# Performance work log

Hardware: AMD Instinct MI355X
Metric: run time of the kernel (lower is better)

## Reference

```python
import jax, jax.numpy as jnp
import numpy as np

DIM = 1024
NUM_HEADS = 16
WINDOW_SIZE = 512
HEAD_DIM = DIM // NUM_HEADS
SCALE = HEAD_DIM ** (-0.5)


def setup_inputs() -> dict:
    key = jax.random.key(0)
    kq, kk, kv = jax.random.split(key, 3)
    shape = (2, NUM_HEADS, 2048, HEAD_DIM)
    q = jax.random.normal(kq, shape, dtype=jnp.float32)
    k = jax.random.normal(kk, shape, dtype=jnp.float32)
    v = jax.random.normal(kv, shape, dtype=jnp.float32)
    return {"q": q, "k": k, "v": v}


def reference(q, k, v):
    B, H, N, D = q.shape
    pos = jnp.arange(N)
    # causal + sliding window: col <= row and col >= row - w + 1
    window_mask = (pos[None, :] <= pos[:, None]) & (pos[None, :] >= pos[:, None] - WINDOW_SIZE + 1)  # (N, N)
    attn = jnp.einsum("bhnd,bhmd->bhnm", q, k) * SCALE  # (B, H, N, N)
    attn = jnp.where(window_mask[None, None], attn, -jnp.inf)
    attn = jax.nn.softmax(attn, axis=-1)
    attn = jnp.nan_to_num(attn, nan=0.0)
    return jnp.einsum("bhnm,bhmd->bhnd", attn, v)
```

## Files before the change

kernel.cpp:

```cpp
#include <hip/hip_runtime.h>
#include <math.h>


#define SEQ 2048
#define HD  64
#define LDR 72

typedef short short8 __attribute__((ext_vector_type(8)));
typedef float f32x4  __attribute__((ext_vector_type(4)));

static __device__ inline unsigned short f2bf(float f){
  union{float f; unsigned u;} un; un.f=f;
  return (unsigned short)((un.u + 0x7FFFu + ((un.u>>16)&1u))>>16);
}
static __device__ inline int swz(int row){ return (row&3)|(((row>>3)&1)<<2); }

static __device__ __forceinline__ void gll16(const unsigned short* g, unsigned short* l){
  __builtin_amdgcn_global_load_lds(
    (const __attribute__((address_space(1))) unsigned int*)(const void*)g,
    (__attribute__((address_space(3))) unsigned int*)(void*)l, 16, 0, 0);
}

__global__ __launch_bounds__(256) void swa_prep(
    const float* __restrict__ k, const float* __restrict__ v,
    unsigned short* __restrict__ Kb, unsigned short* __restrict__ Vtb)
{
  __shared__ unsigned short Vs[64*68];
  const int tid=threadIdx.x, bid=blockIdx.x;
  const long tbase=(long)bid*4096;
  const float C=0.18033688011112042f;

  #pragma unroll
  for(int i=0;i<2;++i){
    int id=i*256+tid, r=id>>3, lc=id&7;
    float4 f0=*(const float4*)(k+tbase+r*64+lc*8);
    float4 f1=*(const float4*)(k+tbase+r*64+lc*8+4);
    unsigned short hh[8];
    hh[0]=f2bf(f0.x*C); hh[1]=f2bf(f0.y*C); hh[2]=f2bf(f0.z*C); hh[3]=f2bf(f0.w*C);
    hh[4]=f2bf(f1.x*C); hh[5]=f2bf(f1.y*C); hh[6]=f2bf(f1.z*C); hh[7]=f2bf(f1.w*C);
    *(uint4*)(Kb+tbase+r*64+(long)((lc^swz(r))*8))=*(uint4*)hh;
  }
  #pragma unroll
  for(int i=0;i<2;++i){
    int id=i*256+tid, r=id>>3, c=id&7;
    int phys=(c^(r>>3))&7;
    float4 f0=*(const float4*)(v+tbase+r*64+c*8);
    float4 f1=*(const float4*)(v+tbase+r*64+c*8+4);
    ushort4 a,b;
    a.x=f2bf(f0.x); a.y=f2bf(f0.y); a.z=f2bf(f0.z); a.w=f2bf(f0.w);
    b.x=f2bf(f1.x); b.y=f2bf(f1.y); b.z=f2bf(f1.z); b.w=f2bf(f1.w);
    *(ushort4*)&Vs[r*68+phys*8]  =a;
    *(ushort4*)&Vs[r*68+phys*8+4]=b;
  }
  __syncthreads();
  #pragma unroll
  for(int i=0;i<2;++i){
    int id=i*256+tid, d=id>>3, lc=id&7;
    unsigned short t8[8];
    #pragma unroll
    for(int e=0;e<8;++e){
      int key=lc*8+e;
      int phys=((d>>3)^lc)&7;
      t8[e]=Vs[key*68 + phys*8 + (d&7)];
    }
    *(uint4*)(Vtb+tbase+d*64+(long)((lc^swz(d))*8))=*(uint4*)t8;
  }
}

__global__ __launch_bounds__(512) void swa_main(
    const float* __restrict__ q,
    const unsigned short* __restrict__ Kb,
    const unsigned short* __restrict__ Vtb,
    float* __restrict__ out)
{
  __shared__ unsigned short Ks[2][4096];
  __shared__ unsigned short Vsh[2][4096];

  const int tid=threadIdx.x, bid=blockIdx.x;
  const int mt=bid&15, bh=bid>>4, m0=mt*128;
  const long base=(long)bh*SEQ*HD;
  const int wv=tid>>6, lane=tid&63, quad=lane>>4, l16=lane&15;
  const int qrow=m0+wv*16+l16;
  const int h=wv>>2;

  short8 qa[2];
  {
    const float* qp=q+base+(long)qrow*HD+quad*8;
    #pragma unroll
    for(int kk=0;kk<2;++kk){
      float4 f0=*(const float4*)(qp+kk*32);
      float4 f1=*(const float4*)(qp+kk*32+4);
      short8 a;
      a[0]=(short)f2bf(f0.x); a[1]=(short)f2bf(f0.y);
      a[2]=(short)f2bf(f0.z); a[3]=(short)f2bf(f0.w);
      a[4]=(short)f2bf(f1.x); a[5]=(short)f2bf(f1.y);
      a[6]=(short)f2bf(f1.z); a[7]=(short)f2bf(f1.w);
      qa[kk]=a;
    }
  }

  const int rbase=8*(l16>>2)+(l16&3);
  const int swk=(l16&3)|(((l16>>2)&1)<<2);
  const int swv=(l16&3)|(((l16>>3)&1)<<2);
  int kaoff[2][4], vboff[2][4];
  #pragma unroll
  for(int kk=0;kk<2;++kk){
    #pragma unroll
    for(int nt=0;nt<4;++nt)
      kaoff[kk][nt]=(rbase+(nt&1)*4+(nt>>1)*32)*64+(((quad+4*kk)^swk)*8);
    #pragma unroll
    for(int dt=0;dt<4;++dt)
      vboff[kk][dt]=(dt*16+l16)*64+(((quad+4*kk)^swv)*8);
  }

  const unsigned short* Kt=Kb +(long)bh*32*4096;
  const unsigned short* Vt=Vtb+(long)bh*32*4096;
  const int seg=tid*8;

  f32x4 oacc[4];
  #pragma unroll
  for(int dt=0;dt<4;++dt) oacc[dt]=(f32x4){0.f,0.f,0.f,0.f};
  float lrun=0.f;

  const int Tb  =2*mt+1;
  const int Tlo =(2*mt>8)?(2*mt-8):0;
  const int myTb=2*mt+h;
  const int myTlo=(myTb>=8)?(myTb-8):0;
  const bool clip=(myTb>=8);

  gll16(Kt+(long)Tlo*4096+seg, &Ks[0][seg]);
  gll16(Vt+(long)Tlo*4096+seg, &Vsh[0][seg]);
  __syncthreads();

  for(int t=Tlo;t<=Tb;++t){
    const int buf=(t-Tlo)&1;
    if(t<Tb){
      gll16(Kt+(long)(t+1)*4096+seg, &Ks[buf^1][seg]);
      gll16(Vt+(long)(t+1)*4096+seg, &Vsh[buf^1][seg]);
    }
    if(t>=myTlo && t<=myTb){
      f32x4 sacc[4];
      #pragma unroll
      for(int nt=0;nt<4;++nt) sacc[nt]=(f32x4){0.f,0.f,0.f,0.f};
      #pragma unroll
      for(int kk=0;kk<2;++kk){
        #pragma unroll
        for(int nt=0;nt<4;++nt){
          short8 ka=*(const short8*)&Ks[buf][kaoff[kk][nt]];
          sacc[nt]=__builtin_amdgcn_mfma_f32_16x16x32_bf16(ka,qa[kk],sacc[nt],0,0,0);
        }
      }
      short8 vb[4][2];
      #pragma unroll
      for(int dt=0;dt<4;++dt)
        #pragma unroll
        for(int kk=0;kk<2;++kk)
          vb[dt][kk]=*(const short8*)&Vsh[buf][vboff[kk][dt]];

      unsigned short pb[16];
      const bool msk=(t==myTb)||(clip&&t==myTlo);
      if(msk){
        #pragma unroll
        for(int nt=0;nt<4;++nt){
          #pragma unroll
          for(int r=0;r<4;++r){
            float e=__builtin_amdgcn_exp2f(sacc[nt][r]);
            int key=t*64+8*quad+r+(nt&1)*4+(nt>>1)*32;
            bool valid=(key<=qrow)&&(key+511>=qrow);
            e=valid?e:0.f;
            lrun+=e;
            pb[nt*4+r]=f2bf(e);
          }
        }
      } else {
        #pragma unroll
        for(int nt=0;nt<4;++nt){
          #pragma unroll
          for(int r=0;r<4;++r){
            float e=__builtin_amdgcn_exp2f(sacc[nt][r]);
            lrun+=e;
            pb[nt*4+r]=f2bf(e);
          }
        }
      }
      short8 pa0,pa1;
      #pragma unroll
      for(int j=0;j<8;++j){ pa0[j]=(short)pb[j]; pa1[j]=(short)pb[8+j]; }
      #pragma unroll
      for(int dt=0;dt<4;++dt){
        oacc[dt]=__builtin_amdgcn_mfma_f32_16x16x32_bf16(pa0,vb[dt][0],oacc[dt],0,0,0);
        oacc[dt]=__builtin_amdgcn_mfma_f32_16x16x32_bf16(pa1,vb[dt][1],oacc[dt],0,0,0);
      }
    }
    __syncthreads();
  }

  lrun+=__shfl_xor(lrun,16);
  lrun+=__shfl_xor(lrun,32);
  float linv=1.0f/lrun;
  #pragma unroll
  for(int r=0;r<4;++r){
    float lr=__shfl(linv,quad*4+r);
    const int orow=m0+wv*16+quad*4+r;
    #pragma unroll
    for(int dt=0;dt<4;++dt)
      out[base+(long)orow*HD+dt*16+l16]=oacc[dt][r]*lr;
  }
}

__global__ __launch_bounds__(256) void swa_fwd(
    const float* __restrict__ q, const float* __restrict__ k,
    const float* __restrict__ v, float* __restrict__ out)
{
  __shared__ short Qs[64*LDR];
  __shared__ short Ps[64*LDR];
  __shared__ short Ksh[2][64*LDR];
  __shared__ short Vtr[2][HD*LDR];

  const int tid=threadIdx.x, bid=blockIdx.x;
  const int mtile=bid&31, bh=bid>>5, m0=mtile*64;
  const long base=(long)bh*SEQ*HD;
  const int wv=tid>>6, lane=tid&63, quad=lane>>4, l16=lane&15;
  const int dcol=lane;

  {
    const float4* qg=(const float4*)(q+base+(long)m0*HD);
    #pragma unroll
    for(int i=0;i<4;++i){
      int idx=i*256+tid, r=idx>>4, c4=idx&15;
      float4 f=qg[idx];
      ushort4 hh; hh.x=f2bf(f.x); hh.y=f2bf(f.y); hh.z=f2bf(f.z); hh.w=f2bf(f.w);
      *(ushort4*)&Qs[r*LDR+c4*4]=hh;
    }
  }
  const int tb=mtile, tlo=(tb>8)?(tb-8):0;
  float4 kreg[4]; float vcol[4][4];
  {
    const float4* kg=(const float4*)(k+base+(long)(tlo*64)*HD);
    const float*  vg=v+base+(long)(tlo*64)*HD;
    #pragma unroll
    for(int i=0;i<4;++i) kreg[i]=kg[i*256+tid];
    #pragma unroll
    for(int g=0;g<4;++g){ int r0=wv*4+g*16;
      #pragma unroll
      for(int j=0;j<4;++j) vcol[g][j]=vg[(r0+j)*HD+dcol]; }
  }
  __syncthreads();
  short8 qa[2];
  #pragma unroll
  for(int kk=0;kk<2;++kk)
    qa[kk]=*(const short8*)&Qs[(wv*16+l16)*LDR+kk*32+quad*8];
  {
    #pragma unroll
    for(int i=0;i<4;++i){
      int idx=i*256+tid, r=idx>>4, c4=idx&15;
      float4 fk=kreg[i];
      ushort4 hk; hk.x=f2bf(fk.x); hk.y=f2bf(fk.y); hk.z=f2bf(fk.z); hk.w=f2bf(fk.w);
      *(ushort4*)&Ksh[0][r*LDR+c4*4]=hk;
    }
    #pragma unroll
    for(int g=0;g<4;++g){ int r0=wv*4+g*16;
      ushort4 hv; hv.x=f2bf(vcol[g][0]); hv.y=f2bf(vcol[g][1]);
                  hv.z=f2bf(vcol[g][2]); hv.w=f2bf(vcol[g][3]);
      *(ushort4*)&Vtr[0][dcol*LDR+r0]=hv; }
  }
  float lrun[4]={0.f,0.f,0.f,0.f};
  f32x4 oacc[4];
  #pragma unroll
  for(int dt=0;dt<4;++dt) oacc[dt]=(f32x4){0.f,0.f,0.f,0.f};
  __syncthreads();

  for(int t=tlo;t<=tb;++t){
    const int buf=(t-tlo)&1, j0=t*64;
    f32x4 sacc[4];
    #pragma unroll
    for(int nt=0;nt<4;++nt) sacc[nt]=(f32x4){0.f,0.f,0.f,0.f};
    #pragma unroll
    for(int kk=0;kk<2;++kk){
      #pragma unroll
      for(int nt=0;nt<4;++nt){
        short8 kb=*(const short8*)&Ksh[buf][(nt*16+l16)*LDR+kk*32+quad*8];
        sacc[nt]=__builtin_amdgcn_mfma_f32_16x16x32_bf16(qa[kk],kb,sacc[nt],0,0,0);
      }
    }
    if(t<tb){
      const float4* kg=(const float4*)(k+base+(long)((t+1)*64)*HD);
      const float*  vg=v+base+(long)((t+1)*64)*HD;
      #pragma unroll
      for(int i=0;i<4;++i) kreg[i]=kg[i*256+tid];
      #pragma unroll
      for(int g=0;g<4;++g){ int r0=wv*4+g*16;
        #pragma unroll
        for(int j=0;j<4;++j) vcol[g][j]=vg[(r0+j)*HD+dcol]; }
    }
    #pragma unroll
    for(int r=0;r<4;++r){
      const int grr=m0+wv*16+quad*4+r;
      #pragma unroll
      for(int nt=0;nt<4;++nt){
        const int gc=j0+nt*16+l16;
        float e=exp2f(sacc[nt][r]*0.18033688011112042f);
        float p=((gc<=grr)&&(gc>=grr-511))?e:0.f;
        lrun[r]+=p;
        Ps[(wv*16+quad*4+r)*LDR+nt*16+l16]=(short)f2bf(p);
      }
    }
    __syncthreads();
    #pragma unroll
    for(int kk=0;kk<2;++kk){
      short8 pa=*(const short8*)&Ps[(wv*16+l16)*LDR+kk*32+quad*8];
      #pragma unroll
      for(int dt=0;dt<4;++dt){
        short8 vb=*(const short8*)&Vtr[buf][(dt*16+l16)*LDR+kk*32+quad*8];
        oacc[dt]=__builtin_amdgcn_mfma_f32_16x16x32_bf16(pa,vb,oacc[dt],0,0,0);
      }
    }
    if(t<tb){
      #pragma unroll
      for(int i=0;i<4;++i){
        int idx=i*256+tid, r=idx>>4, c4=idx&15;
        float4 fk=kreg[i];
        ushort4 hk; hk.x=f2bf(fk.x); hk.y=f2bf(fk.y); hk.z=f2bf(fk.z); hk.w=f2bf(fk.w);
        *(ushort4*)&Ksh[buf^1][r*LDR+c4*4]=hk;
      }
      #pragma unroll
      for(int g=0;g<4;++g){ int r0=wv*4+g*16;
        ushort4 hv; hv.x=f2bf(vcol[g][0]); hv.y=f2bf(vcol[g][1]);
                    hv.z=f2bf(vcol[g][2]); hv.w=f2bf(vcol[g][3]);
        *(ushort4*)&Vtr[buf^1][dcol*LDR+r0]=hv; }
    }
    __syncthreads();
  }
  #pragma unroll
  for(int r=0;r<4;++r){
    float s=lrun[r];
    s+=__shfl_xor(s,1); s+=__shfl_xor(s,2); s+=__shfl_xor(s,4); s+=__shfl_xor(s,8);
    lrun[r]=(s>0.f)?(1.f/s):0.f;
  }
  #pragma unroll
  for(int r=0;r<4;++r){
    const int row=m0+wv*16+quad*4+r;
    #pragma unroll
    for(int dt=0;dt<4;++dt)
      out[base+(long)row*HD+dt*16+l16]=oacc[dt][r]*lrun[r];
  }
}

extern "C" void kernel_launch(void* const* d_in, const int* in_sizes, int n_in,
                              void* d_out, int out_size, void* d_ws, size_t ws_size,
                              hipStream_t stream) {
  (void)in_sizes; (void)n_in; (void)out_size;
  const float* q=(const float*)d_in[0];
  const float* k=(const float*)d_in[1];
  const float* v=(const float*)d_in[2];
  float* o=(float*)d_out;
  const size_t NEED = 2ull*32*2048*64*2;
  if (ws_size>=NEED){
    unsigned short* Kb =(unsigned short*)d_ws;
    unsigned short* Vtb=Kb+32ull*2048*64;
    hipLaunchKernelGGL(swa_prep, dim3(1024), dim3(256), 0, stream, k, v, Kb, Vtb);
    hipLaunchKernelGGL(swa_main, dim3(512),  dim3(512), 0, stream, q, Kb, Vtb, o);
  } else {
    hipLaunchKernelGGL(swa_fwd, dim3(1024), dim3(256), 0, stream, q, k, v, o);
  }
}
```

Baseline: 110.0 us.

## Process two key tiles per barrier and split prep kernel into K and V blocks

The main attention loop now stages two 64-key tiles of K and V per double-buffered stage, which halves the number of __syncthreads barriers and issues larger batches of async global-to-LDS loads. LDS use grows to 64KB per block, which may limit occupancy. The prep kernel now launches separate blocks for K conversion and V transpose, doubling the grid so the two jobs run in parallel and only the V blocks need shared memory. The tile count per block is even (10 or 2*mt+2), so the pairing covers every tile.

```diff
diff --git a/kernel.cpp b/kernel.cpp
--- a/kernel.cpp
+++ b/kernel.cpp
@@ -25,45 +25,49 @@
     const float* __restrict__ k, const float* __restrict__ v,
     unsigned short* __restrict__ Kb, unsigned short* __restrict__ Vtb)
 {
-  __shared__ unsigned short Vs[64*68];
   const int tid=threadIdx.x, bid=blockIdx.x;
-  const long tbase=(long)bid*4096;
   const float C=0.18033688011112042f;
 
-  #pragma unroll
-  for(int i=0;i<2;++i){
-    int id=i*256+tid, r=id>>3, lc=id&7;
-    float4 f0=*(const float4*)(k+tbase+r*64+lc*8);
-    float4 f1=*(const float4*)(k+tbase+r*64+lc*8+4);
-    unsigned short hh[8];
-    hh[0]=f2bf(f0.x*C); hh[1]=f2bf(f0.y*C); hh[2]=f2bf(f0.z*C); hh[3]=f2bf(f0.w*C);
-    hh[4]=f2bf(f1.x*C); hh[5]=f2bf(f1.y*C); hh[6]=f2bf(f1.z*C); hh[7]=f2bf(f1.w*C);
-    *(uint4*)(Kb+tbase+r*64+(long)((lc^swz(r))*8))=*(uint4*)hh;
-  }
-  #pragma unroll
-  for(int i=0;i<2;++i){
-    int id=i*256+tid, r=id>>3, c=id&7;
-    int phys=(c^(r>>3))&7;
-    float4 f0=*(const float4*)(v+tbase+r*64+c*8);
-    float4 f1=*(const float4*)(v+tbase+r*64+c*8+4);
-    ushort4 a,b;
-    a.x=f2bf(f0.x); a.y=f2bf(f0.y); a.z=f2bf(f0.z); a.w=f2bf(f0.w);
-    b.x=f2bf(f1.x); b.y=f2bf(f1.y); b.z=f2bf(f1.z); b.w=f2bf(f1.w);
-    *(ushort4*)&Vs[r*68+phys*8]  =a;
-    *(ushort4*)&Vs[r*68+phys*8+4]=b;
-  }
-  __syncthreads();
-  #pragma unroll
-  for(int i=0;i<2;++i){
-    int id=i*256+tid, d=id>>3, lc=id&7;
-    unsigned short t8[8];
-    #pragma unroll
-    for(int e=0;e<8;++e){
-      int key=lc*8+e;
-      int phys=((d>>3)^lc)&7;
-      t8[e]=Vs[key*68 + phys*8 + (d&7)];
-    }
-    *(uint4*)(Vtb+tbase+d*64+(long)((lc^swz(d))*8))=*(uint4*)t8;
+  if(bid<1024){
+    const long tbase=(long)bid*4096;
+    #pragma unroll
+    for(int i=0;i<2;++i){
+      int id=i*256+tid, r=id>>3, lc=id&7;
+      float4 f0=*(const float4*)(k+tbase+r*64+lc*8);
+      float4 f1=*(const float4*)(k+tbase+r*64+lc*8+4);
+      unsigned short hh[8];
+      hh[0]=f2bf(f0.x*C); hh[1]=f2bf(f0.y*C); hh[2]=f2bf(f0.z*C); hh[3]=f2bf(f0.w*C);
+      hh[4]=f2bf(f1.x*C); hh[5]=f2bf(f1.y*C); hh[6]=f2bf(f1.z*C); hh[7]=f2bf(f1.w*C);
+      *(uint4*)(Kb+tbase+r*64+(long)((lc^swz(r))*8))=*(uint4*)hh;
+    }
+  } else {
+    __shared__ unsigned short Vs[64*68];
+    const long tbase=(long)(bid-1024)*4096;
+    #pragma unroll
+    for(int i=0;i<2;++i){
+      int id=i*256+tid, r=id>>3, c=id&7;
+      int phys=(c^(r>>3))&7;
+      float4 f0=*(const float4*)(v+tbase+r*64+c*8);
+      float4 f1=*(const float4*)(v+tbase+r*64+c*8+4);
+      ushort4 a,b;
+      a.x=f2bf(f0.x); a.y=f2bf(f0.y); a.z=f2bf(f0.z); a.w=f2bf(f0.w);
+      b.x=f2bf(f1.x); b.y=f2bf(f1.y); b.z=f2bf(f1.z); b.w=f2bf(f1.w);
+      *(ushort4*)&Vs[r*68+phys*8]  =a;
+      *(ushort4*)&Vs[r*68+phys*8+4]=b;
+    }
+    __syncthreads();
+    #pragma unroll
+    for(int i=0;i<2;++i){
+      int id=i*256+tid, d=id>>3, lc=id&7;
+      unsigned short t8[8];
+      #pragma unroll
+      for(int e=0;e<8;++e){
+        int key=lc*8+e;
+        int phys=((d>>3)^lc)&7;
+        t8[e]=Vs[key*68 + phys*8 + (d&7)];
+      }
+      *(uint4*)(Vtb+tbase+d*64+(long)((lc^swz(d))*8))=*(uint4*)t8;
+    }
   }
 }
 
@@ -73,8 +77,8 @@
     const unsigned short* __restrict__ Vtb,
     float* __restrict__ out)
 {
-  __shared__ unsigned short Ks[2][4096];
-  __shared__ unsigned short Vsh[2][4096];
+  __shared__ unsigned short Ks[2][8192];
+  __shared__ unsigned short Vsh[2][8192];
 
   const int tid=threadIdx.x, bid=blockIdx.x;
   const int mt=bid&15, bh=bid>>4, m0=mt*128;
@@ -124,72 +128,86 @@
 
   const int Tb  =2*mt+1;
   const int Tlo =(2*mt>8)?(2*mt-8):0;
+  const int npairs=(Tb-Tlo+1)>>1;
   const int myTb=2*mt+h;
   const int myTlo=(myTb>=8)?(myTb-8):0;
   const bool clip=(myTb>=8);
 
-  gll16(Kt+(long)Tlo*4096+seg, &Ks[0][seg]);
-  gll16(Vt+(long)Tlo*4096+seg, &Vsh[0][seg]);
+  {
+    const long o=(long)Tlo*4096;
+    gll16(Kt+o+seg,      &Ks[0][seg]);
+    gll16(Kt+o+4096+seg, &Ks[0][4096+seg]);
+    gll16(Vt+o+seg,      &Vsh[0][seg]);
+    gll16(Vt+o+4096+seg, &Vsh[0][4096+seg]);
+  }
   __syncthreads();
 
-  for(int t=Tlo;t<=Tb;++t){
-    const int buf=(t-Tlo)&1;
-    if(t<Tb){
-      gll16(Kt+(long)(t+1)*4096+seg, &Ks[buf^1][seg]);
-      gll16(Vt+(long)(t+1)*4096+seg, &Vsh[buf^1][seg]);
-    }
-    if(t>=myTlo && t<=myTb){
-      f32x4 sacc[4];
-      #pragma unroll
-      for(int nt=0;nt<4;++nt) sacc[nt]=(f32x4){0.f,0.f,0.f,0.f};
-      #pragma unroll
-      for(int kk=0;kk<2;++kk){
-        #pragma unroll
-        for(int nt=0;nt<4;++nt){
-          short8 ka=*(const short8*)&Ks[buf][kaoff[kk][nt]];
-          sacc[nt]=__builtin_amdgcn_mfma_f32_16x16x32_bf16(ka,qa[kk],sacc[nt],0,0,0);
-        }
-      }
-      short8 vb[4][2];
-      #pragma unroll
-      for(int dt=0;dt<4;++dt)
-        #pragma unroll
-        for(int kk=0;kk<2;++kk)
-          vb[dt][kk]=*(const short8*)&Vsh[buf][vboff[kk][dt]];
-
-      unsigned short pb[16];
-      const bool msk=(t==myTb)||(clip&&t==myTlo);
-      if(msk){
-        #pragma unroll
-        for(int nt=0;nt<4;++nt){
+  for(int p=0;p<npairs;++p){
+    const int buf=p&1;
+    if(p+1<npairs){
+      const long o=(long)(Tlo+2*(p+1))*4096;
+      gll16(Kt+o+seg,      &Ks[buf^1][seg]);
+      gll16(Kt+o+4096+seg, &Ks[buf^1][4096+seg]);
+      gll16(Vt+o+seg,      &Vsh[buf^1][seg]);
+      gll16(Vt+o+4096+seg, &Vsh[buf^1][4096+seg]);
+    }
+    #pragma unroll
+    for(int sub=0;sub<2;++sub){
+      const int t=Tlo+2*p+sub;
+      if(t>=myTlo && t<=myTb){
+        const int tb_off=sub*4096;
+        f32x4 sacc[4];
+        #pragma unroll
+        for(int nt=0;nt<4;++nt) sacc[nt]=(f32x4){0.f,0.f,0.f,0.f};
+        #pragma unroll
+        for(int kk=0;kk<2;++kk){
           #pragma unroll
-          for(int r=0;r<4;++r){
-            float e=__builtin_amdgcn_exp2f(sacc[nt][r]);
-            int key=t*64+8*quad+r+(nt&1)*4+(nt>>1)*32;
-            bool valid=(key<=qrow)&&(key+511>=qrow);
-            e=valid?e:0.f;
-            lrun+=e;
-            pb[nt*4+r]=f2bf(e);
+          for(int nt=0;nt<4;++nt){
+            short8 ka=*(const short8*)&Ks[buf][tb_off+kaoff[kk][nt]];
+            sacc[nt]=__builtin_amdgcn_mfma_f32_16x16x32_bf16(ka,qa[kk],sacc[nt],0,0,0);
           }
         }
-      } else {
-        #pragma unroll
-        for(int nt=0;nt<4;++nt){
+        short8 vb[4][2];
+        #pragma unroll
+        for(int dt=0;dt<4;++dt)
           #pragma unroll
-          for(int r=0;r<4;++r){
-            float e=__builtin_amdgcn_exp2f(sacc[nt][r]);
-            lrun+=e;
-            pb[nt*4+r]=f2bf(e);
+          for(int kk=0;kk<2;++kk)
+            vb[dt][kk]=*(const short8*)&Vsh[buf][tb_off+vboff[kk][dt]];
+
+        unsigned short pb[16];
+        const bool msk=(t==myTb)||(clip&&t==myTlo);
+        if(msk){
+          #pragma unroll
+          for(int nt=0;nt<4;++nt){
+            #pragma unroll
+            for(int r=0;r<4;++r){
+              float e=__builtin_amdgcn_exp2f(sacc[nt][r]);
+              int key=t*64+8*quad+r+(nt&1)*4+(nt>>1)*32;
+              bool valid=(key<=qrow)&&(key+511>=qrow);
+              e=valid?e:0.f;
+              lrun+=e;
+              pb[nt*4+r]=f2bf(e);
+            }
+          }
+        } else {
+          #pragma unroll
+          for(int nt=0;nt<4;++nt){
+            #pragma unroll
+            for(int r=0;r<4;++r){
+              float e=__builtin_amdgcn_exp2f(sacc[nt][r]);
+              lrun+=e;
+              pb[nt*4+r]=f2bf(e);
+            }
           }
         }
-      }
-      short8 pa0,pa1;
-      #pragma unroll
-      for(int j=0;j<8;++j){ pa0[j]=(short)pb[j]; pa1[j]=(short)pb[8+j]; }
-      #pragma unroll
-      for(int dt=0;dt<4;++dt){
-        oacc[dt]=__builtin_amdgcn_mfma_f32_16x16x32_bf16(pa0,vb[dt][0],oacc[dt],0,0,0);
-        oacc[dt]=__builtin_amdgcn_mfma_f32_16x16x32_bf16(pa1,vb[dt][1],oacc[dt],0,0,0);
+        short8 pa0,pa1;
+        #pragma unroll
+        for(int j=0;j<8;++j){ pa0[j]=(short)pb[j]; pa1[j]=(short)pb[8+j]; }
+        #pragma unroll
+        for(int dt=0;dt<4;++dt){
+          oacc[dt]=__builtin_amdgcn_mfma_f32_16x16x32_bf16(pa0,vb[dt][0],oacc[dt],0,0,0);
+          oacc[dt]=__builtin_amdgcn_mfma_f32_16x16x32_bf16(pa1,vb[dt][1],oacc[dt],0,0,0);
+        }
       }
     }
     __syncthreads();
@@ -358,7 +376,7 @@
   if (ws_size>=NEED){
     unsigned short* Kb =(unsigned short*)d_ws;
     unsigned short* Vtb=Kb+32ull*2048*64;
-    hipLaunchKernelGGL(swa_prep, dim3(1024), dim3(256), 0, stream, k, v, Kb, Vtb);
+    hipLaunchKernelGGL(swa_prep, dim3(2048), dim3(256), 0, stream, k, v, Kb, Vtb);
     hipLaunchKernelGGL(swa_main, dim3(512),  dim3(512), 0, stream, q, Kb, Vtb, o);
   } else {
     hipLaunchKernelGGL(swa_fwd, dim3(1024), dim3(256), 0, stream, q, k, v, o);
```

Result: no change. 112.0 us (+1.8%).
